# Kernel tuning notes

Hardware: AMD Instinct MI355X
Metric: run time of the kernel (lower is better)

## Reference

```python
import jax, jax.numpy as jnp
import numpy as np

NEG_INF = jnp.float32(-1e30)
EPS = 1e-7  # keras.backend.ctc_batch_cost epsilon


def ctc_batch_cost(y_true, y_pred):
    """Faithful CTC loss (keras ctc_batch_cost semantics): y_pred are
    probabilities [B,T,C], blank = C-1, full input/label lengths.
    Returns per-example negative log likelihood [B,1]."""
    B, T, C = y_pred.shape
    L = y_true.shape[1]
    S = 2 * L + 1  # extended label length (blanks interleaved)
    blank = C - 1

    log_probs = jnp.log(y_pred + EPS)  # [B,T,C]

    # Extended label sequence: blank, l0, blank, l1, ..., blank  -> [B,S]
    ext = jnp.full((B, S), blank, dtype=y_true.dtype)
    ext = ext.at[:, 1::2].set(y_true)

    # Skip transition allowed at s if ext[s] != blank and ext[s] != ext[s-2]
    skip = jnp.concatenate(
        [jnp.zeros((B, 2), dtype=bool),
         (ext[:, 2:] != blank) & (ext[:, 2:] != ext[:, :-2])], axis=1)  # [B,S]

    # Gather log-probs of extended labels per timestep: [T,B,S]
    lp_ext = jnp.take_along_axis(log_probs, ext[:, None, :], axis=2)  # [B,T,S]
    lp_ext = jnp.transpose(lp_ext, (1, 0, 2))  # [T,B,S]

    # alpha init at t=0: only positions 0 (blank) and 1 (first label)
    alpha0 = jnp.full((B, S), NEG_INF, dtype=log_probs.dtype)
    alpha0 = alpha0.at[:, 0].set(lp_ext[0, :, 0])
    alpha0 = alpha0.at[:, 1].set(lp_ext[0, :, 1])

    pad1 = jnp.full((B, 1), NEG_INF, dtype=log_probs.dtype)
    pad2 = jnp.full((B, 2), NEG_INF, dtype=log_probs.dtype)

    def step(alpha, lp_t):
        a_stay = alpha
        a_prev = jnp.concatenate([pad1, alpha[:, :-1]], axis=1)
        a_skip = jnp.where(skip, jnp.concatenate([pad2, alpha[:, :-2]], axis=1), NEG_INF)
        m = jnp.maximum(jnp.maximum(a_stay, a_prev), a_skip)
        lse = m + jnp.log(jnp.exp(a_stay - m) + jnp.exp(a_prev - m) + jnp.exp(a_skip - m))
        return lse + lp_t, None

    alpha_T, _ = jax.lax.scan(step, alpha0, lp_ext[1:])  # [B,S]

    # log P = logsumexp over last blank and last label positions
    end = jnp.stack([alpha_T[:, S - 1], alpha_T[:, S - 2]], axis=1)  # [B,2]
    loglik = jax.nn.logsumexp(end, axis=1)  # [B]
    return -loglik[:, None]  # [B,1] like keras ctc_batch_cost


def setup_inputs() -> dict:
    key = jax.random.key(0)
    k1, k2 = jax.random.split(key)
    B, T, C, L = 512, 512, 128, 32
    y_true = jax.random.randint(k1, (B, L), 0, C - 1, dtype=jnp.int64 if jax.config.read('jax_enable_x64') else jnp.int32)
    y_pred = jax.random.uniform(k2, (B, T, C), dtype=jnp.float32)
    return {"y_true": y_true, "y_pred": y_pred}


def reference(y_true, y_pred):
    return ctc_batch_cost(y_true, y_pred)
```

## Files before the change

### kernel.cpp

```cpp
#include <hip/hip_runtime.h>


#define EPSF 1e-7f

constexpr int C_  = 128;
constexpr int L_  = 32;
constexpr int PFG = 4;

__device__ __forceinline__ float wshr1(float x) {
    return __int_as_float(
        __builtin_amdgcn_mov_dpp(__float_as_int(x), 0x138, 0xf, 0xf, true));
}

__device__ __forceinline__ int sample_eb(float v) {
    int mb = __builtin_amdgcn_readlane(__float_as_int(v), 3);
#pragma unroll
    for (int i = 1; i < 16; ++i) {
        const int t = __builtin_amdgcn_readlane(__float_as_int(v), 4 * i + 3);
        mb = (t > mb) ? t : mb;
    }
    const int eb = (int)((unsigned)mb >> 23);
    return (eb > 27) ? eb : 27;
}

__launch_bounds__(128)
__global__ void ctc_loss_kernel(const int* __restrict__ y_true,
                                const float* __restrict__ y_pred,
                                float* __restrict__ out) {
    __shared__ float shR[65];
    __shared__ int   shE;

    const int b    = blockIdx.x;
    const int tid  = threadIdx.x;
    const int lane = tid & 63;
    const int w    = tid >> 6;

    const float* bb  = y_pred + (size_t)b * 512 * C_;
    const int*   lbl = y_true + b * L_;

    int   cls0 = C_ - 1;
    float sg0  = 0.f;
    if (w == 0) {
        if (lane & 1) cls0 = lbl[(lane - 1) >> 1];
        if ((lane & 1) && lane >= 3) {
            const int li = (lane - 1) >> 1;
            if (lbl[li] != lbl[li - 1]) sg0 = 1.f;
        }
    } else {
        if (lane & 1) cls0 = lbl[31 - ((lane - 1) >> 1)];
        if ((lane & 1) && lane >= 3) {
            const int li = (lane - 1) >> 1;
            if (lbl[31 - li] != lbl[32 - li]) sg0 = 1.f;
        }
    }

    auto rowp = [&](int t) {
        const int orig = w ? (511 - t) : t;
        return bb + (size_t)orig * C_ + cls0;
    };
    const int rs = w ? -C_ : C_;

    float a       = (lane < 2) ? (rowp(0)[0] + EPSF) : 0.f;
    float a64     = 0.f;
    int   e_total = 0;

    auto loadQ = [&](float (&Pk)[4], int g) {
        const float* r = rowp(1 + 4 * g);
        Pk[0] = r[0]; Pk[1] = r[rs]; Pk[2] = r[2 * rs]; Pk[3] = r[3 * rs];
    };

    auto group4 = [&](const float (&P)[4]) {
        float x = a, z = a64;
#pragma unroll
        for (int r = 0; r < 4; ++r) {
            const float q  = P[r] + EPSF;
            const float qs = wshr1(q);
            const float x1 = wshr1(x);
            const float x2 = wshr1(x1);
            z = (z + x) * qs;
            x = (x + x1 + sg0 * x2) * q;
        }
        a = x; a64 = z;
    };

    auto scale = [&](int eb) {
        e_total += eb - 127;
        const float inv = __uint_as_float((unsigned)(254 - eb) << 23);
        a *= inv; a64 *= inv;
    };

    float Q[PFG][4];
#pragma unroll
    for (int k = 0; k < PFG; ++k) loadQ(Q[k], k);
    int ebp = sample_eb(a);

#pragma clang loop unroll(disable)
    for (int gq = 0; gq < 15; ++gq) {
#pragma unroll
        for (int k = 0; k < PFG; ++k) {
            group4(Q[k]);
            scale(ebp);
            ebp = sample_eb(a);
            int gn = gq * PFG + k + PFG;
            if (gn > 62) gn = 62;
            loadQ(Q[k], gn);
        }
    }

    float qo[3];
#pragma unroll
    for (int r = 0; r < 3; ++r) qo[r] = rowp(253 + r)[0];

#pragma unroll
    for (int k = 0; k < 3; ++k) {
        group4(Q[k]);
        scale(ebp);
        if (k < 2) ebp = sample_eb(a);
    }

#pragma unroll
    for (int r = 0; r < 3; ++r) {
        const float p1 = wshr1(a);
        const float p2 = wshr1(p1);
        const float qb = wshr1(qo[r]);
        const float an = (a + p1 + sg0 * p2) * (qo[r] + EPSF);
        a64 = (a64 + a) * (qb + EPSF);
        a = an;
    }

    if (w == 1) {
        shR[lane] = a;
        if (lane == 63) shR[64] = a64;
        if (lane == 0)  shE = e_total;
    }
    __syncthreads();

    if (w == 0) {
        const float a1 = wshr1(a);
        const float a2 = wshr1(a1);
        const float abar = a + a1 + sg0 * a2;
        double p = (double)abar * (double)shR[64 - lane];
        if (lane == 63) p += (double)(a64 + a) * (double)shR[0];
#pragma unroll
        for (int m = 1; m < 64; m <<= 1) p += __shfl(p, lane ^ m);
        if (lane == 0) {
            if (p < 1e-300) p = 1e-300;
            const unsigned long long bt = __double_as_longlong(p);
            const int k = (int)((bt >> 52) & 0x7FFULL) - 1023;
            const double mant = __longlong_as_double(
                (bt & 0x000FFFFFFFFFFFFFULL) | 0x3FF0000000000000ULL);
            out[b] = -(__logf((float)mant) +
                       (float)(e_total + shE + k) * 0.6931471805599453f);
        }
    }
}

extern "C" void kernel_launch(void* const* d_in, const int* in_sizes, int n_in,
                              void* d_out, int out_size, void* d_ws, size_t ws_size,
                              hipStream_t stream) {
    const int*   y_true = (const int*)d_in[0];
    const float* y_pred = (const float*)d_in[1];
    float*       out    = (float*)d_out;

    const int B = out_size;
    ctc_loss_kernel<<<B, 128, 0, stream>>>(y_true, y_pred, out);
}
```

Before: 191.8 us.

## Add coalesced cache-warming row loads ahead of the CTC recurrence

Adds coalesced full-row loads of y_pred rows eight groups ahead of use, so the later scattered per-lane gather loads hit in cache instead of waiting on DRAM. The main loop is re-tiled to eight groups per iteration, with the four-deep gather pipeline indexed modulo four and a longer tail. The warm loads are kept alive through an empty asm sink. This adds extra load instructions and registers per thread, which could lower occupancy or contend with the gather loads.

```diff
diff --git a/kernel.cpp b/kernel.cpp
--- a/kernel.cpp
+++ b/kernel.cpp
@@ -69,6 +69,13 @@
         Pk[0] = r[0]; Pk[1] = r[rs]; Pk[2] = r[2 * rs]; Pk[3] = r[3 * rs];
     };
 
+    auto warm = [&](float& A, float& B, int g) {
+        const int r0 = w ? (507 - 4 * g) : (1 + 4 * g);
+        const float* p = bb + (size_t)r0 * C_ + lane * 4;
+        A = p[0];
+        B = p[256];
+    };
+
     auto group4 = [&](const float (&P)[4]) {
         float x = a, z = a64;
 #pragma unroll
@@ -89,21 +96,28 @@
         a *= inv; a64 *= inv;
     };
 
+    float Wa[8], Wb[8];
+    float wsum = 0.f;
+#pragma unroll
+    for (int k = 0; k < 8; ++k) warm(Wa[k], Wb[k], k);
+
     float Q[PFG][4];
 #pragma unroll
     for (int k = 0; k < PFG; ++k) loadQ(Q[k], k);
     int ebp = sample_eb(a);
 
 #pragma clang loop unroll(disable)
-    for (int gq = 0; gq < 15; ++gq) {
+    for (int gq = 0; gq < 7; ++gq) {
 #pragma unroll
-        for (int k = 0; k < PFG; ++k) {
-            group4(Q[k]);
+        for (int k = 0; k < 8; ++k) {
+            const int g = gq * 8 + k;
+            wsum += Wa[k] + Wb[k];
+            group4(Q[k & 3]);
             scale(ebp);
             ebp = sample_eb(a);
-            int gn = gq * PFG + k + PFG;
-            if (gn > 62) gn = 62;
-            loadQ(Q[k], gn);
+            loadQ(Q[k & 3], g + 4);
+            int gw = g + 8; if (gw > 62) gw = 62;
+            warm(Wa[k], Wb[k], gw);
         }
     }
 
@@ -112,11 +126,14 @@
     for (int r = 0; r < 3; ++r) qo[r] = rowp(253 + r)[0];
 
 #pragma unroll
-    for (int k = 0; k < 3; ++k) {
-        group4(Q[k]);
+    for (int j = 0; j < 7; ++j) {
+        wsum += Wa[j] + Wb[j];
+        group4(Q[j & 3]);
         scale(ebp);
-        if (k < 2) ebp = sample_eb(a);
+        if (j < 6) ebp = sample_eb(a);
+        if (j < 3) loadQ(Q[j & 3], 60 + j);
     }
+    wsum += Wa[7] + Wb[7];
 
 #pragma unroll
     for (int r = 0; r < 3; ++r) {
@@ -153,6 +170,8 @@
                        (float)(e_total + shE + k) * 0.6931471805599453f);
         }
     }
+
+    asm volatile("" :: "v"(wsum));
 }
 
 extern "C" void kernel_launch(void* const* d_in, const int* in_sizes, int n_in,
```

New measurement: 199.9 us. 4.2% more time.

## Stage per-example label probabilities into LDS table via async global-to-LDS loads

Applied to the files above, without the earlier changes.

Before the recursion starts, the kernel streams every y_pred row for the example through a small LDS ring using global_load_lds. It gathers the 33 needed class columns (32 labels plus blank) into a [512][36] shared table. The alpha recursion then reads probabilities from LDS instead of issuing scattered, latency-bound global loads on the serial critical path. The trade-off is an extra serialized preload phase with two barriers per chunk and about 74KB of LDS per block, which lowers occupancy.

```diff
diff --git a/kernel.cpp b/kernel.cpp
--- a/kernel.cpp
+++ b/kernel.cpp
@@ -3,9 +3,9 @@
 
 #define EPSF 1e-7f
 
-constexpr int C_  = 128;
-constexpr int L_  = 32;
-constexpr int PFG = 4;
+constexpr int C_    = 128;
+constexpr int L_    = 32;
+constexpr int NSLOT = 36;
 
 __device__ __forceinline__ float wshr1(float x) {
     return __int_as_float(
@@ -23,10 +23,19 @@
     return (eb > 27) ? eb : 27;
 }
 
+__device__ __forceinline__ void gl16(const float* gp, float* lp) {
+    __builtin_amdgcn_global_load_lds(
+        (const __attribute__((address_space(1))) void*)gp,
+        (__attribute__((address_space(3))) void*)lp,
+        16, 0, 0);
+}
+
 __launch_bounds__(128)
 __global__ void ctc_loss_kernel(const int* __restrict__ y_true,
                                 const float* __restrict__ y_pred,
                                 float* __restrict__ out) {
+    __shared__ float table[512][NSLOT];
+    __shared__ float ring[8][128];
     __shared__ float shR[65];
     __shared__ int   shE;
 
@@ -38,35 +47,55 @@
     const float* bb  = y_pred + (size_t)b * 512 * C_;
     const int*   lbl = y_true + b * L_;
 
-    int   cls0 = C_ - 1;
-    float sg0  = 0.f;
+    const int s0 = tid % NSLOT;
+    const int r0 = tid / NSLOT;
+    const int c0 = (s0 < 32) ? lbl[s0] : (C_ - 1);
+    const int s1 = 20 + tid;
+    const int c1 = (tid < 12) ? lbl[s1] : (C_ - 1);
+
+    int   slot;
+    float sg0 = 0.f;
     if (w == 0) {
-        if (lane & 1) cls0 = lbl[(lane - 1) >> 1];
+        slot = (lane & 1) ? ((lane - 1) >> 1) : 32;
         if ((lane & 1) && lane >= 3) {
             const int li = (lane - 1) >> 1;
             if (lbl[li] != lbl[li - 1]) sg0 = 1.f;
         }
     } else {
-        if (lane & 1) cls0 = lbl[31 - ((lane - 1) >> 1)];
+        slot = (lane & 1) ? (31 - ((lane - 1) >> 1)) : 32;
         if ((lane & 1) && lane >= 3) {
             const int li = (lane - 1) >> 1;
             if (lbl[31 - li] != lbl[32 - li]) sg0 = 1.f;
         }
     }
 
-    auto rowp = [&](int t) {
-        const int orig = w ? (511 - t) : t;
-        return bb + (size_t)orig * C_ + cls0;
+    auto issue = [&](int c) {
+        const int row = c * 4 + w * 2;
+        gl16(bb + (size_t)row * C_ + lane * 4, &ring[row & 7][0]);
     };
-    const int rs = w ? -C_ : C_;
+    issue(0); issue(1);
+#pragma clang loop unroll(disable)
+    for (int c = 0; c < 128; ++c) {
+        if (c < 127) asm volatile("s_waitcnt vmcnt(1)" ::: "memory");
+        else         asm volatile("s_waitcnt vmcnt(0)" ::: "memory");
+        __syncthreads();
+        const int rb = c * 4;
+        if (s0 < 33)  table[rb + r0][s0] = ring[(rb + r0) & 7][c0];
+        if (tid < 13) table[rb + 3][s1]  = ring[(rb + 3) & 7][c1];
+        __syncthreads();
+        if (c + 2 < 128) issue(c + 2);
+    }
 
-    float a       = (lane < 2) ? (rowp(0)[0] + EPSF) : 0.f;
+    auto trow = [&](int t) { return w ? (511 - t) : t; };
+
+    float a       = (lane < 2) ? (table[trow(0)][slot] + EPSF) : 0.f;
     float a64     = 0.f;
     int   e_total = 0;
 
-    auto loadQ = [&](float (&Pk)[4], int g) {
-        const float* r = rowp(1 + 4 * g);
-        Pk[0] = r[0]; Pk[1] = r[rs]; Pk[2] = r[2 * rs]; Pk[3] = r[3 * rs];
+    auto ldsq = [&](float (&Pk)[4], int g) {
+        const int t0 = 1 + 4 * g;
+#pragma unroll
+        for (int j = 0; j < 4; ++j) Pk[j] = table[trow(t0 + j)][slot];
     };
 
     auto group4 = [&](const float (&P)[4]) {
@@ -89,41 +118,25 @@
         a *= inv; a64 *= inv;
     };
 
-    float Q[PFG][4];
-#pragma unroll
-    for (int k = 0; k < PFG; ++k) loadQ(Q[k], k);
+    float Q[2][4];
+    ldsq(Q[0], 0); ldsq(Q[1], 1);
     int ebp = sample_eb(a);
 
 #pragma clang loop unroll(disable)
-    for (int gq = 0; gq < 15; ++gq) {
-#pragma unroll
-        for (int k = 0; k < PFG; ++k) {
-            group4(Q[k]);
-            scale(ebp);
-            ebp = sample_eb(a);
-            int gn = gq * PFG + k + PFG;
-            if (gn > 62) gn = 62;
-            loadQ(Q[k], gn);
-        }
-    }
-
-    float qo[3];
-#pragma unroll
-    for (int r = 0; r < 3; ++r) qo[r] = rowp(253 + r)[0];
-
-#pragma unroll
-    for (int k = 0; k < 3; ++k) {
-        group4(Q[k]);
+    for (int g = 0; g < 63; ++g) {
+        group4(Q[g & 1]);
         scale(ebp);
-        if (k < 2) ebp = sample_eb(a);
+        ebp = sample_eb(a);
+        if (g + 2 < 63) ldsq(Q[g & 1], g + 2);
     }
 
 #pragma unroll
     for (int r = 0; r < 3; ++r) {
+        const float qo = table[trow(253 + r)][slot];
         const float p1 = wshr1(a);
         const float p2 = wshr1(p1);
-        const float qb = wshr1(qo[r]);
-        const float an = (a + p1 + sg0 * p2) * (qo[r] + EPSF);
+        const float qb = wshr1(qo);
+        const float an = (a + p1 + sg0 * p2) * (qo + EPSF);
         a64 = (a64 + a) * (qb + EPSF);
         a = an;
     }
```

Measured after the change: 283.6 us. 1.48x slower.
